# Optimization experiments

Hardware: AMD Instinct MI355X
Metric: run time of the kernel (lower is better)

## Reference

```python
import jax, jax.numpy as jnp
import numpy as np

EXPAND = 2  # expand_ratio: head dim


def setup_inputs() -> dict:
    key = jax.random.key(0)
    k1, k2, k3 = jax.random.split(key, 3)
    n, b, d = 4096, 8, 1024
    x = jax.random.normal(k1, (n, b, d), dtype=jnp.float32)
    lower_bound = jnp.zeros((d,), dtype=jnp.float32)
    W_in = jax.random.normal(k2, (d, 3 * d), dtype=jnp.float32) / np.sqrt(d)
    W_out = jax.random.normal(k3, (d, d), dtype=jnp.float32) / np.sqrt(d)
    return {"x": x, "lower_bound": lower_bound, "W_in": W_in, "W_out": W_out}


def reference(x, lower_bound, W_in, W_out):
    # x: (n, b, d) sequence-first
    n, b, d = x.shape
    e = EXPAND
    h = d // e
    feat = x @ W_in                                  # (n, b, 3d)
    V, Q, Fg = jnp.split(feat, 3, axis=-1)
    V = jax.nn.gelu(V, approximate=False)            # nn.GELU default = exact erf
    Q = jax.nn.gelu(Q, approximate=False)
    Fg = jax.nn.sigmoid(Fg)
    V = V.reshape(n, b, h, e)
    Q = Q.reshape(n, b, h, e)
    Fg = Fg.reshape(n, b, h, e)
    lb = lower_bound.reshape(h, e)
    lam = lb + (1.0 - lb) * Fg                       # decay gate in (lb, 1)
    K = 1.0 - lam
    # GLA recurrence: S_t = diag(lam_t) S_{t-1} + k_t v_t^T ; o_t = q_t S_t
    # (exp(log_lambda) == lambda, so log-space decay collapses to direct multiply)
    def step(S, inp):
        lam_t, k_t, v_t, q_t = inp                   # each (b, h, e)
        S = lam_t[..., :, None] * S + k_t[..., :, None] * v_t[..., None, :]
        o_t = jnp.einsum('bhk,bhkv->bhv', q_t, S)
        return S, o_t
    S0 = jnp.zeros((b, h, e, e), dtype=x.dtype)
    _, o = jax.lax.scan(step, S0, (lam, K, V, Q))    # o: (n, b, h, e)
    o = o.reshape(n, b, d)
    return o @ W_out
```

## Files before the change

kernel.cpp:

```cpp
#include <hip/hip_runtime.h>
#include <hip/hip_bf16.h>
#include <math.h>

using frag8 = __attribute__((ext_vector_type(8))) short;
using f32x4 = __attribute__((ext_vector_type(4))) float;

#define BM 256
#define BN 256

typedef const __attribute__((address_space(1))) unsigned char glb_u8;
typedef __attribute__((address_space(3))) unsigned char lds_u8;

__device__ __forceinline__ float b2f(unsigned short v) {
    union { unsigned u; float f; } x; x.u = ((unsigned)v) << 16; return x.f;
}
__device__ __forceinline__ unsigned short f2b(float f) {
    union { float f; unsigned u; } x; x.f = f;
    unsigned u = x.u;
    u += 0x7fffu + ((u >> 16) & 1u);
    return (unsigned short)(u >> 16);
}

__global__ __launch_bounds__(256) void cast_kernel(const float* __restrict__ in,
                                                   unsigned short* __restrict__ out, long n) {
    long i = ((long)blockIdx.x * 256 + threadIdx.x) * 8;
    if (i >= n) return;
    float4 a = *(const float4*)(in + i);
    float4 b = *(const float4*)(in + i + 4);
    struct alignas(16) U8 { unsigned short s[8]; } o;
    o.s[0] = f2b(a.x); o.s[1] = f2b(a.y); o.s[2] = f2b(a.z); o.s[3] = f2b(a.w);
    o.s[4] = f2b(b.x); o.s[5] = f2b(b.y); o.s[6] = f2b(b.z); o.s[7] = f2b(b.w);
    *(U8*)(out + i) = o;
}

__global__ void transpose_cast(const float* __restrict__ in, unsigned short* __restrict__ out,
                               int R, int Ccols) {
    __shared__ float tile[32][33];
    int bx = blockIdx.x * 32;
    int by = blockIdx.y * 32;
    int tx = threadIdx.x, ty = threadIdx.y;
    for (int r = ty; r < 32; r += 8)
        tile[r][tx] = in[(size_t)(by + r) * Ccols + bx + tx];
    __syncthreads();
    for (int r = ty; r < 32; r += 8)
        out[(size_t)(bx + r) * R + by + tx] = f2b(tile[tx][r]);
}

__global__ __launch_bounds__(512, 2) void gemm_bf16(
    const unsigned short* __restrict__ A, const unsigned short* __restrict__ Bt,
    int M, int N, int K, int mode,
    float* __restrict__ Cf,
    unsigned short* __restrict__ Vp, unsigned short* __restrict__ Qp,
    unsigned short* __restrict__ Lp, const float* __restrict__ lb) {
    __shared__ __align__(16) char smem[131072];

    const int tid = threadIdx.x;
    const int lane16 = tid & 15;
    const int quad = (tid >> 4) & 3;
    const int wave = tid >> 6;
    const int wm = wave >> 2;
    const int wn = wave & 3;

    const int nbx = N / BN;
    const int nwg = (int)gridDim.x;
    const int sw = ((int)blockIdx.x & 7) * (nwg >> 3) + ((int)blockIdx.x >> 3);
    const long m0 = (long)(sw / nbx) * BM;
    const long n0 = (long)(sw % nbx) * BN;
    const long K2 = (long)K * 2;

    const int c0 = (tid & 7) ^ ((tid >> 3) & 7);
    long srcL0, srcL1; int dstL0, dstL1;
    {
        const int kk2 = (c0 & 3) << 4;
        const int r0 = ((tid >> 3) << 1) + (c0 >> 2);
        const int r1 = ((64 + (tid >> 3)) << 1) + (c0 >> 2);
        srcL0 = (long)r0 * K2 + kk2;
        srcL1 = (long)r1 * K2 + kk2;
        dstL0 = tid * 16;
        dstL1 = 8192 + tid * 16;
    }
    const char* Ab = (const char*)A + m0 * K2;
    const char* Bb = (const char*)Bt + n0 * K2;

    int offA[8], offB[4];
#pragma unroll
    for (int mf = 0; mf < 8; ++mf) {
        int row = wm * 128 + mf * 16 + lane16;
        int line = row >> 1;
        int c = (((row & 1) << 2) | quad) ^ (line & 7);
        offA[mf] = line * 128 + c * 16;
    }
#pragma unroll
    for (int nf = 0; nf < 4; ++nf) {
        int row = wn * 64 + nf * 16 + lane16;
        int line = row >> 1;
        int c = (((row & 1) << 2) | quad) ^ (line & 7);
        offB[nf] = 16384 + line * 128 + c * 16;
    }

    f32x4 acc[8][4];
#pragma unroll
    for (int i = 0; i < 8; ++i)
#pragma unroll
        for (int j = 0; j < 4; ++j) acc[i][j] = (f32x4){0.f, 0.f, 0.f, 0.f};

#define STAGE(u) do { \
        char* ldb = smem + ((u) & 3) * 32768; \
        long kb = (long)(u) * 64; \
        __builtin_amdgcn_global_load_lds((glb_u8*)(Ab + srcL0 + kb), (lds_u8*)(ldb + dstL0), 16, 0, 0); \
        __builtin_amdgcn_global_load_lds((glb_u8*)(Ab + srcL1 + kb), (lds_u8*)(ldb + dstL1), 16, 0, 0); \
        __builtin_amdgcn_global_load_lds((glb_u8*)(Bb + srcL0 + kb), (lds_u8*)(ldb + 16384 + dstL0), 16, 0, 0); \
        __builtin_amdgcn_global_load_lds((glb_u8*)(Bb + srcL1 + kb), (lds_u8*)(ldb + 16384 + dstL1), 16, 0, 0); \
    } while (0)

    const int NT = K >> 5;
    STAGE(0); STAGE(1); STAGE(2);
    asm volatile("s_waitcnt vmcnt(8)" ::: "memory");
    __builtin_amdgcn_s_barrier();

    for (int t = 0; t < NT; ++t) {
        if (t + 3 < NT) STAGE(t + 3);
        const char* ub = smem + (t & 3) * 32768;
        frag8 bfr[4], af[4];
#pragma unroll
        for (int nf = 0; nf < 4; ++nf) bfr[nf] = *(const frag8*)(ub + offB[nf]);
#pragma unroll
        for (int mf = 0; mf < 4; ++mf) af[mf] = *(const frag8*)(ub + offA[mf]);
        __builtin_amdgcn_s_setprio(1);
#pragma unroll
        for (int mf = 0; mf < 4; ++mf)
#pragma unroll
            for (int nf = 0; nf < 4; ++nf)
                acc[mf][nf] = __builtin_amdgcn_mfma_f32_16x16x32_bf16(af[mf], bfr[nf], acc[mf][nf], 0, 0, 0);
        __builtin_amdgcn_s_setprio(0);
#pragma unroll
        for (int mf = 0; mf < 4; ++mf) af[mf] = *(const frag8*)(ub + offA[4 + mf]);
        __builtin_amdgcn_s_setprio(1);
#pragma unroll
        for (int mf = 0; mf < 4; ++mf)
#pragma unroll
            for (int nf = 0; nf < 4; ++nf)
                acc[4 + mf][nf] = __builtin_amdgcn_mfma_f32_16x16x32_bf16(af[mf], bfr[nf], acc[4 + mf][nf], 0, 0, 0);
        __builtin_amdgcn_s_setprio(0);
        if (t < NT - 3)       { asm volatile("s_waitcnt vmcnt(8)" ::: "memory"); }
        else if (t == NT - 3) { asm volatile("s_waitcnt vmcnt(4)" ::: "memory"); }
        else if (t == NT - 2) { asm volatile("s_waitcnt vmcnt(0)" ::: "memory"); }
        __builtin_amdgcn_s_barrier();
    }
#undef STAGE

    if (mode == 0) {
#pragma unroll
        for (int mf = 0; mf < 8; ++mf)
#pragma unroll
            for (int nf = 0; nf < 4; ++nf) {
                long col = n0 + wn * 64 + nf * 16 + lane16;
#pragma unroll
                for (int r = 0; r < 4; ++r) {
                    long row = m0 + wm * 128 + mf * 16 + quad * 4 + r;
                    Cf[row * N + col] = acc[mf][nf][r];
                }
            }
    } else {
        const int seg = (int)(n0 >> 10);
        const int cbase = (int)(n0 & 1023) + wn * 64;
        unsigned short* dst = (seg == 0) ? Vp : (seg == 1 ? Qp : Lp);
#pragma unroll
        for (int mf = 0; mf < 8; ++mf)
#pragma unroll
            for (int nf = 0; nf < 4; ++nf) {
                int col = cbase + nf * 16 + lane16;
#pragma unroll
                for (int r = 0; r < 4; ++r) {
                    long row = m0 + wm * 128 + mf * 16 + quad * 4 + r;
                    float v = acc[mf][nf][r];
                    float res;
                    if (seg < 2) {
                        float u = 1.59576912f * v * (1.0f + 0.044715f * v * v);
                        res = v / (1.0f + __expf(-u));
                    } else {
                        float sg = 1.0f / (1.0f + __expf(-v));
                        float l = lb[col];
                        res = l + (1.0f - l) * sg;
                    }
                    dst[row * 1024 + col] = f2b(res);
                }
            }
    }
}

__global__ __launch_bounds__(256) void scan_phase1(
    const unsigned short* __restrict__ lam, const unsigned short* __restrict__ V,
    float* __restrict__ Sl, float* __restrict__ P, int L) {
    int cid = blockIdx.x * 256 + threadIdx.x;
    int c = blockIdx.y;
    int bi = cid >> 9, h = cid & 511;
    float s00 = 0, s01 = 0, s10 = 0, s11 = 0, p0 = 1.f, p1 = 1.f;
    int t0 = c * L;
    const unsigned* lamp = (const unsigned*)lam;
    const unsigned* vp = (const unsigned*)V;
    for (int t = t0; t < t0 + L; ++t) {
        long idx = (long)(t * 8 + bi) * 512 + h;
        unsigned lu = lamp[idx], vu = vp[idx];
        float la0 = b2f((unsigned short)lu), la1 = b2f((unsigned short)(lu >> 16));
        float v0 = b2f((unsigned short)vu), v1 = b2f((unsigned short)(vu >> 16));
        float k0 = 1.f - la0, k1 = 1.f - la1;
        s00 = fmaf(la0, s00, k0 * v0); s01 = fmaf(la0, s01, k0 * v1);
        s10 = fmaf(la1, s10, k1 * v0); s11 = fmaf(la1, s11, k1 * v1);
        p0 *= la0; p1 *= la1;
    }
    long base = (long)c * 4096 + cid;
    ((float4*)Sl)[base] = make_float4(s00, s01, s10, s11);
    ((float2*)P)[base] = make_float2(p0, p1);
}

__global__ __launch_bounds__(256) void scan_phase2(
    const float* __restrict__ Sl, const float* __restrict__ P,
    float* __restrict__ Sini, int C) {
    int idx = blockIdx.x * 256 + threadIdx.x;
    int cid = idx >> 2, ij = idx & 3, i = (idx >> 1) & 1;
    float s = 0.f;
    for (int c = 0; c < C; ++c) {
        long base = (long)c * 4096 + cid;
        Sini[base * 4 + ij] = s;
        s = fmaf(P[base * 2 + i], s, Sl[base * 4 + ij]);
    }
}

__global__ __launch_bounds__(256) void scan_phase3(
    const unsigned short* __restrict__ lam, const unsigned short* __restrict__ V,
    const unsigned short* __restrict__ Q, const float* __restrict__ Sini,
    unsigned short* __restrict__ o, int L) {
    int cid = blockIdx.x * 256 + threadIdx.x;
    int c = blockIdx.y;
    int bi = cid >> 9, h = cid & 511;
    float4 si = ((const float4*)Sini)[(long)c * 4096 + cid];
    float s00 = si.x, s01 = si.y, s10 = si.z, s11 = si.w;
    int t0 = c * L;
    const unsigned* lamp = (const unsigned*)lam;
    const unsigned* vp = (const unsigned*)V;
    const unsigned* qp = (const unsigned*)Q;
    unsigned* op = (unsigned*)o;
    for (int t = t0; t < t0 + L; ++t) {
        long idx = (long)(t * 8 + bi) * 512 + h;
        unsigned lu = lamp[idx], vu = vp[idx], qu = qp[idx];
        float la0 = b2f((unsigned short)lu), la1 = b2f((unsigned short)(lu >> 16));
        float v0 = b2f((unsigned short)vu), v1 = b2f((unsigned short)(vu >> 16));
        float q0 = b2f((unsigned short)qu), q1 = b2f((unsigned short)(qu >> 16));
        float k0 = 1.f - la0, k1 = 1.f - la1;
        s00 = fmaf(la0, s00, k0 * v0); s01 = fmaf(la0, s01, k0 * v1);
        s10 = fmaf(la1, s10, k1 * v0); s11 = fmaf(la1, s11, k1 * v1);
        float o0 = q0 * s00 + q1 * s10;
        float o1 = q0 * s01 + q1 * s11;
        op[idx] = (unsigned)f2b(o0) | ((unsigned)f2b(o1) << 16);
    }
}

extern "C" void kernel_launch(void* const* d_in, const int* in_sizes, int n_in,
                              void* d_out, int out_size, void* d_ws, size_t ws_size,
                              hipStream_t stream) {
    const float* x = (const float*)d_in[0];
    const float* lb = (const float*)d_in[1];
    const float* W_in = (const float*)d_in[2];
    const float* W_out = (const float*)d_in[3];
    float* out = (float*)d_out;

    const int n = 4096, b = 8, d = 1024;
    const long NB = (long)n * b;
    const int C = 64, L = 64;

    char* ws = (char*)d_ws;
    size_t off = 0;
    auto alloc = [&](size_t bytes) -> char* {
        char* p = ws + off;
        off += (bytes + 255) & ~(size_t)255;
        return p;
    };
    unsigned short* xb   = (unsigned short*)alloc(NB * d * 2);
    unsigned short* Wint = (unsigned short*)alloc((size_t)3 * d * d * 2);
    unsigned short* Wot  = (unsigned short*)alloc((size_t)d * d * 2);
    unsigned short* Vb   = (unsigned short*)alloc(NB * d * 2);
    unsigned short* Qb   = (unsigned short*)alloc(NB * d * 2);
    unsigned short* Lb   = (unsigned short*)alloc(NB * d * 2);
    float* Sl   = (float*)alloc((size_t)C * 4096 * 4 * 4);
    float* P    = (float*)alloc((size_t)C * 4096 * 2 * 4);
    float* Sini = (float*)alloc((size_t)C * 4096 * 4 * 4);

    cast_kernel<<<dim3((unsigned)((NB * d) / (256 * 8))), 256, 0, stream>>>(x, xb, NB * d);
    transpose_cast<<<dim3(3 * d / 32, d / 32), dim3(32, 8), 0, stream>>>(W_in, Wint, d, 3 * d);
    transpose_cast<<<dim3(d / 32, d / 32), dim3(32, 8), 0, stream>>>(W_out, Wot, d, d);
    const int nwg1 = (3 * d / BN) * (int)(NB / BM);
    gemm_bf16<<<dim3(nwg1), 512, 0, stream>>>(
        xb, Wint, (int)NB, 3 * d, d, 1, nullptr, Vb, Qb, Lb, lb);
    scan_phase1<<<dim3(16, C), 256, 0, stream>>>(Lb, Vb, Sl, P, L);
    scan_phase2<<<dim3(64), 256, 0, stream>>>(Sl, P, Sini, C);
    unsigned short* ob = xb;
    scan_phase3<<<dim3(16, C), 256, 0, stream>>>(Lb, Vb, Qb, Sini, ob, L);
    const int nwg2 = (d / BN) * (int)(NB / BM);
    gemm_bf16<<<dim3(nwg2), 512, 0, stream>>>(
        ob, Wot, (int)NB, d, d, 0, out, nullptr, nullptr, nullptr, nullptr);
}
```

Measured before the change: 711.2 us.

## Restructure GEMM main loop into fine-grained 8-phase ping-pong schedule

Replaces the 4-stage K=32 LDS ring with two 64 KB buffers, each holding a K=64 tile split into A and B quarter-tiles. Loads are issued one quarter at a time, interleaved with LDS fragment reads and MFMA blocks separated by barriers. The loop is unrolled over K=128, and the LDS layout and swizzle change accordingly. The goal is finer overlap of global→LDS loads, LDS reads and MFMA, at the cost of many more barriers and an assumption that K is a multiple of 128.

```diff
diff --git a/kernel.cpp b/kernel.cpp
--- a/kernel.cpp
+++ b/kernel.cpp
@@ -68,86 +68,116 @@
     const long n0 = (long)(sw % nbx) * BN;
     const long K2 = (long)K * 2;
 
-    const int c0 = (tid & 7) ^ ((tid >> 3) & 7);
-    long srcL0, srcL1; int dstL0, dstL1;
-    {
-        const int kk2 = (c0 & 3) << 4;
-        const int r0 = ((tid >> 3) << 1) + (c0 >> 2);
-        const int r1 = ((64 + (tid >> 3)) << 1) + (c0 >> 2);
-        srcL0 = (long)r0 * K2 + kk2;
-        srcL1 = (long)r1 * K2 + kk2;
-        dstL0 = tid * 16;
-        dstL1 = 8192 + tid * 16;
-    }
+    const int c16 = (((tid & 7) ^ ((tid >> 3) & 7)) << 4);
+    const long o64 = 64 * K2, o128 = 128 * K2;
     const char* Ab = (const char*)A + m0 * K2;
     const char* Bb = (const char*)Bt + n0 * K2;
-
-    int offA[8], offB[4];
-#pragma unroll
-    for (int mf = 0; mf < 8; ++mf) {
-        int row = wm * 128 + mf * 16 + lane16;
-        int line = row >> 1;
-        int c = (((row & 1) << 2) | quad) ^ (line & 7);
-        offA[mf] = line * 128 + c * 16;
-    }
-#pragma unroll
-    for (int nf = 0; nf < 4; ++nf) {
-        int row = wn * 64 + nf * 16 + lane16;
-        int line = row >> 1;
-        int c = (((row & 1) << 2) | quad) ^ (line & 7);
-        offB[nf] = 16384 + line * 128 + c * 16;
-    }
+    const char* pA0 = Ab + (long)(tid >> 3) * K2 + c16;
+    const char* pA1 = pA0 + o128;
+    const char* pB0 = Bb + (long)(tid >> 3) * K2 + c16;
+    const char* pB1 = pB0 + o128;
+    const int dst0 = tid * 16;
+
+    const int baseA = wm * 16384 + lane16 * 128;
+    const int baseB = 32768 + (wn >> 1) * 16384 + (wn & 1) * 8192 + lane16 * 128;
+    const int swz0 = ((quad ^ (lane16 & 7)) << 4);
+    const int swz1 = (((4 + quad) ^ (lane16 & 7)) << 4);
 
     f32x4 acc[8][4];
 #pragma unroll
     for (int i = 0; i < 8; ++i)
 #pragma unroll
         for (int j = 0; j < 4; ++j) acc[i][j] = (f32x4){0.f, 0.f, 0.f, 0.f};
-
-#define STAGE(u) do { \
-        char* ldb = smem + ((u) & 3) * 32768; \
-        long kb = (long)(u) * 64; \
-        __builtin_amdgcn_global_load_lds((glb_u8*)(Ab + srcL0 + kb), (lds_u8*)(ldb + dstL0), 16, 0, 0); \
-        __builtin_amdgcn_global_load_lds((glb_u8*)(Ab + srcL1 + kb), (lds_u8*)(ldb + dstL1), 16, 0, 0); \
-        __builtin_amdgcn_global_load_lds((glb_u8*)(Bb + srcL0 + kb), (lds_u8*)(ldb + 16384 + dstL0), 16, 0, 0); \
-        __builtin_amdgcn_global_load_lds((glb_u8*)(Bb + srcL1 + kb), (lds_u8*)(ldb + 16384 + dstL1), 16, 0, 0); \
+    frag8 a0[4], a1[4], b0[4], b1[4];
+
+#define STAGE(P, R, KO) do { \
+        __builtin_amdgcn_global_load_lds((glb_u8*)((P) + (KO)), \
+            (lds_u8*)(smem + (R) + dst0), 16, 0, 0); \
+        __builtin_amdgcn_global_load_lds((glb_u8*)((P) + o64 + (KO)), \
+            (lds_u8*)(smem + (R) + 8192 + dst0), 16, 0, 0); \
     } while (0)
-
-    const int NT = K >> 5;
-    STAGE(0); STAGE(1); STAGE(2);
-    asm volatile("s_waitcnt vmcnt(8)" ::: "memory");
-    __builtin_amdgcn_s_barrier();
-
-    for (int t = 0; t < NT; ++t) {
-        if (t + 3 < NT) STAGE(t + 3);
-        const char* ub = smem + (t & 3) * 32768;
-        frag8 bfr[4], af[4];
-#pragma unroll
-        for (int nf = 0; nf < 4; ++nf) bfr[nf] = *(const frag8*)(ub + offB[nf]);
-#pragma unroll
-        for (int mf = 0; mf < 4; ++mf) af[mf] = *(const frag8*)(ub + offA[mf]);
-        __builtin_amdgcn_s_setprio(1);
-#pragma unroll
-        for (int mf = 0; mf < 4; ++mf)
-#pragma unroll
-            for (int nf = 0; nf < 4; ++nf)
-                acc[mf][nf] = __builtin_amdgcn_mfma_f32_16x16x32_bf16(af[mf], bfr[nf], acc[mf][nf], 0, 0, 0);
-        __builtin_amdgcn_s_setprio(0);
-#pragma unroll
-        for (int mf = 0; mf < 4; ++mf) af[mf] = *(const frag8*)(ub + offA[4 + mf]);
-        __builtin_amdgcn_s_setprio(1);
-#pragma unroll
-        for (int mf = 0; mf < 4; ++mf)
-#pragma unroll
-            for (int nf = 0; nf < 4; ++nf)
-                acc[4 + mf][nf] = __builtin_amdgcn_mfma_f32_16x16x32_bf16(af[mf], bfr[nf], acc[4 + mf][nf], 0, 0, 0);
-        __builtin_amdgcn_s_setprio(0);
-        if (t < NT - 3)       { asm volatile("s_waitcnt vmcnt(8)" ::: "memory"); }
-        else if (t == NT - 3) { asm volatile("s_waitcnt vmcnt(4)" ::: "memory"); }
-        else if (t == NT - 2) { asm volatile("s_waitcnt vmcnt(0)" ::: "memory"); }
-        __builtin_amdgcn_s_barrier();
-    }
+#define RD4(D, BUF, BASE, SW) do { \
+        D[0] = *(const frag8*)(smem + (BUF) + (BASE) + (SW)); \
+        D[1] = *(const frag8*)(smem + (BUF) + (BASE) + 2048 + (SW)); \
+        D[2] = *(const frag8*)(smem + (BUF) + (BASE) + 4096 + (SW)); \
+        D[3] = *(const frag8*)(smem + (BUF) + (BASE) + 6144 + (SW)); \
+    } while (0)
+#define MM(AF, BF, RO) do { \
+        _Pragma("unroll") \
+        for (int _m = 0; _m < 4; ++_m) \
+            _Pragma("unroll") \
+            for (int _n = 0; _n < 4; ++_n) \
+                acc[(RO) + _m][_n] = __builtin_amdgcn_mfma_f32_16x16x32_bf16( \
+                    AF[_m], BF[_n], acc[(RO) + _m][_n], 0, 0, 0); \
+    } while (0)
+#define VM2 asm volatile("s_waitcnt vmcnt(2)" ::: "memory")
+#define VM0 asm volatile("s_waitcnt vmcnt(0)" ::: "memory")
+#define BARR __builtin_amdgcn_s_barrier()
+#define PRIO1 __builtin_amdgcn_s_setprio(1)
+#define PRIO0 __builtin_amdgcn_s_setprio(0)
+
+    STAGE(pA0, 0, 0); STAGE(pA1, 16384, 0); STAGE(pB0, 32768, 0); STAGE(pB1, 49152, 0);
+    STAGE(pA0, 65536, 128);
+    VM2; BARR;
+    RD4(a0, 0, baseA, swz0); RD4(b0, 0, baseB, swz0);
+
+    long ko = 0;
+    const int NI = K >> 7;
+    for (int i = 0; i < NI - 1; ++i, ko += 256) {
+        STAGE(pA1, 65536 + 16384, ko + 128);
+        RD4(a1, 0, baseA + 8192, swz0);
+        BARR; PRIO1; MM(a0, b0, 0); PRIO0; BARR;
+        STAGE(pB0, 65536 + 32768, ko + 128);
+        RD4(a0, 0, baseA, swz1); RD4(b1, 0, baseB, swz1);
+        BARR; PRIO1; MM(a1, b0, 4); PRIO0; BARR;
+        STAGE(pB1, 65536 + 49152, ko + 128);
+        RD4(a1, 0, baseA + 8192, swz1);
+        BARR; PRIO1; MM(a0, b1, 0); PRIO0; BARR;
+        STAGE(pA0, 0, ko + 256);
+        VM2; BARR;
+        RD4(a0, 65536, baseA, swz0); RD4(b0, 65536, baseB, swz0);
+        PRIO1; MM(a1, b1, 4); PRIO0; BARR;
+        STAGE(pA1, 16384, ko + 256);
+        RD4(a1, 65536, baseA + 8192, swz0);
+        BARR; PRIO1; MM(a0, b0, 0); PRIO0; BARR;
+        STAGE(pB0, 32768, ko + 256);
+        RD4(a0, 65536, baseA, swz1); RD4(b1, 65536, baseB, swz1);
+        BARR; PRIO1; MM(a1, b0, 4); PRIO0; BARR;
+        STAGE(pB1, 49152, ko + 256);
+        RD4(a1, 65536, baseA + 8192, swz1);
+        BARR; PRIO1; MM(a0, b1, 0); PRIO0; BARR;
+        STAGE(pA0, 65536, ko + 384);
+        VM2; BARR;
+        RD4(a0, 0, baseA, swz0); RD4(b0, 0, baseB, swz0);
+        PRIO1; MM(a1, b1, 4); PRIO0; BARR;
+    }
+    STAGE(pA1, 65536 + 16384, ko + 128);
+    RD4(a1, 0, baseA + 8192, swz0);
+    BARR; PRIO1; MM(a0, b0, 0); PRIO0; BARR;
+    STAGE(pB0, 65536 + 32768, ko + 128);
+    RD4(a0, 0, baseA, swz1); RD4(b1, 0, baseB, swz1);
+    BARR; PRIO1; MM(a1, b0, 4); PRIO0; BARR;
+    STAGE(pB1, 65536 + 49152, ko + 128);
+    RD4(a1, 0, baseA + 8192, swz1);
+    BARR; PRIO1; MM(a0, b1, 0); PRIO0; BARR;
+    VM0; BARR;
+    RD4(a0, 65536, baseA, swz0); RD4(b0, 65536, baseB, swz0);
+    PRIO1; MM(a1, b1, 4); PRIO0; BARR;
+    RD4(a1, 65536, baseA + 8192, swz0);
+    BARR; PRIO1; MM(a0, b0, 0); PRIO0; BARR;
+    RD4(a0, 65536, baseA, swz1); RD4(b1, 65536, baseB, swz1);
+    BARR; PRIO1; MM(a1, b0, 4); PRIO0; BARR;
+    RD4(a1, 65536, baseA + 8192, swz1);
+    BARR; PRIO1; MM(a0, b1, 0); PRIO0; BARR;
+    PRIO1; MM(a1, b1, 4); PRIO0;
 #undef STAGE
+#undef RD4
+#undef MM
+#undef VM2
+#undef VM0
+#undef BARR
+#undef PRIO1
+#undef PRIO0
 
     if (mode == 0) {
 #pragma unroll
```

Measured after the change: 706.7 us. About the same (-0.6%).

## Restructure bf16 GEMM main loop into ping-pong register double-buffered schedule

Applied to the files above, without the earlier changes.

Rewrites the GEMM inner loop to process two K-steps per iteration. It splits the A and B global-to-LDS staging into separate phases and prefetches the next tile's A/B fragments into alternate register sets while MFMAs run on the current ones. It also changes the LDS layout to a simpler row-major tile with a 4-way XOR swizzle and precomputed base read offsets. The intent is to overlap LDS reads and global loads with MFMA work, at the cost of more barriers per step, higher register pressure, and a loop that assumes an even number of K steps.

```diff
diff --git a/kernel.cpp b/kernel.cpp
--- a/kernel.cpp
+++ b/kernel.cpp
@@ -55,8 +55,9 @@
     __shared__ __align__(16) char smem[131072];
 
     const int tid = threadIdx.x;
-    const int lane16 = tid & 15;
-    const int quad = (tid >> 4) & 3;
+    const int lane = tid & 63;
+    const int lane16 = lane & 15;
+    const int quad = lane >> 4;
     const int wave = tid >> 6;
     const int wm = wave >> 2;
     const int wn = wave & 3;
@@ -68,86 +69,105 @@
     const long n0 = (long)(sw % nbx) * BN;
     const long K2 = (long)K * 2;
 
-    const int c0 = (tid & 7) ^ ((tid >> 3) & 7);
-    long srcL0, srcL1; int dstL0, dstL1;
-    {
-        const int kk2 = (c0 & 3) << 4;
-        const int r0 = ((tid >> 3) << 1) + (c0 >> 2);
-        const int r1 = ((64 + (tid >> 3)) << 1) + (c0 >> 2);
-        srcL0 = (long)r0 * K2 + kk2;
-        srcL1 = (long)r1 * K2 + kk2;
-        dstL0 = tid * 16;
-        dstL1 = 8192 + tid * 16;
-    }
+    const int c0x16 = (((tid & 3) ^ ((tid >> 3) & 3)) << 4);
+    const long srcO0 = (long)(tid >> 2) * K2 + c0x16;
+    const long srcO1 = srcO0 + 128 * K2;
     const char* Ab = (const char*)A + m0 * K2;
     const char* Bb = (const char*)Bt + n0 * K2;
-
-    int offA[8], offB[4];
-#pragma unroll
-    for (int mf = 0; mf < 8; ++mf) {
-        int row = wm * 128 + mf * 16 + lane16;
-        int line = row >> 1;
-        int c = (((row & 1) << 2) | quad) ^ (line & 7);
-        offA[mf] = line * 128 + c * 16;
-    }
-#pragma unroll
-    for (int nf = 0; nf < 4; ++nf) {
-        int row = wn * 64 + nf * 16 + lane16;
-        int line = row >> 1;
-        int c = (((row & 1) << 2) | quad) ^ (line & 7);
-        offB[nf] = 16384 + line * 128 + c * 16;
-    }
+    const int dst0 = tid * 16;
+
+    const int swz = ((quad ^ ((lane16 >> 1) & 3)) << 4);
+    const int aRd = wm * 8192 + lane16 * 64 + swz;
+    const int bRd = 16384 + wn * 4096 + lane16 * 64 + swz;
 
     f32x4 acc[8][4];
 #pragma unroll
     for (int i = 0; i < 8; ++i)
 #pragma unroll
         for (int j = 0; j < 4; ++j) acc[i][j] = (f32x4){0.f, 0.f, 0.f, 0.f};
-
-#define STAGE(u) do { \
-        char* ldb = smem + ((u) & 3) * 32768; \
-        long kb = (long)(u) * 64; \
-        __builtin_amdgcn_global_load_lds((glb_u8*)(Ab + srcL0 + kb), (lds_u8*)(ldb + dstL0), 16, 0, 0); \
-        __builtin_amdgcn_global_load_lds((glb_u8*)(Ab + srcL1 + kb), (lds_u8*)(ldb + dstL1), 16, 0, 0); \
-        __builtin_amdgcn_global_load_lds((glb_u8*)(Bb + srcL0 + kb), (lds_u8*)(ldb + 16384 + dstL0), 16, 0, 0); \
-        __builtin_amdgcn_global_load_lds((glb_u8*)(Bb + srcL1 + kb), (lds_u8*)(ldb + 16384 + dstL1), 16, 0, 0); \
+    frag8 aL[4], aH[4], bE[4], bO[4];
+
+#define STAGE_A(u_) do { int _sb = ((u_) & 3) << 15; long _kb = (long)(u_) * 64; \
+        __builtin_amdgcn_global_load_lds((glb_u8*)(Ab + srcO0 + _kb), \
+            (lds_u8*)(smem + _sb + dst0), 16, 0, 0); \
+        __builtin_amdgcn_global_load_lds((glb_u8*)(Ab + srcO1 + _kb), \
+            (lds_u8*)(smem + _sb + 8192 + dst0), 16, 0, 0); \
     } while (0)
+#define STAGE_B(u_) do { int _sb = ((u_) & 3) << 15; long _kb = (long)(u_) * 64; \
+        __builtin_amdgcn_global_load_lds((glb_u8*)(Bb + srcO0 + _kb), \
+            (lds_u8*)(smem + _sb + 16384 + dst0), 16, 0, 0); \
+        __builtin_amdgcn_global_load_lds((glb_u8*)(Bb + srcO1 + _kb), \
+            (lds_u8*)(smem + _sb + 24576 + dst0), 16, 0, 0); \
+    } while (0)
+#define RD_ALO(D, u_) do { const char* _p = smem + (((u_) & 3) << 15) + aRd; \
+        D[0] = *(const frag8*)(_p);        D[1] = *(const frag8*)(_p + 1024); \
+        D[2] = *(const frag8*)(_p + 2048); D[3] = *(const frag8*)(_p + 3072); } while (0)
+#define RD_AHI(D, u_) do { const char* _p = smem + (((u_) & 3) << 15) + aRd + 4096; \
+        D[0] = *(const frag8*)(_p);        D[1] = *(const frag8*)(_p + 1024); \
+        D[2] = *(const frag8*)(_p + 2048); D[3] = *(const frag8*)(_p + 3072); } while (0)
+#define RD_B(D, u_) do { const char* _p = smem + (((u_) & 3) << 15) + bRd; \
+        D[0] = *(const frag8*)(_p);        D[1] = *(const frag8*)(_p + 1024); \
+        D[2] = *(const frag8*)(_p + 2048); D[3] = *(const frag8*)(_p + 3072); } while (0)
+#define MM4(AF, BF, RO) do { \
+        _Pragma("unroll") \
+        for (int _m = 0; _m < 4; ++_m) \
+            _Pragma("unroll") \
+            for (int _n = 0; _n < 4; ++_n) \
+                acc[(RO) + _m][_n] = __builtin_amdgcn_mfma_f32_16x16x32_bf16( \
+                    AF[_m], BF[_n], acc[(RO) + _m][_n], 0, 0, 0); \
+    } while (0)
+#define FENCE(x_) do { \
+        if ((x_) < NT - 3)       asm volatile("s_waitcnt vmcnt(8)" ::: "memory"); \
+        else if ((x_) == NT - 3) asm volatile("s_waitcnt vmcnt(4)" ::: "memory"); \
+        else                     asm volatile("s_waitcnt vmcnt(0)" ::: "memory"); \
+    } while (0)
+#define BARR __builtin_amdgcn_s_barrier()
+#define PRIO1 __builtin_amdgcn_s_setprio(1)
+#define PRIO0 __builtin_amdgcn_s_setprio(0)
 
     const int NT = K >> 5;
-    STAGE(0); STAGE(1); STAGE(2);
+
+    STAGE_A(0); STAGE_B(0); STAGE_A(1); STAGE_B(1); STAGE_A(2); STAGE_B(2);
     asm volatile("s_waitcnt vmcnt(8)" ::: "memory");
-    __builtin_amdgcn_s_barrier();
-
-    for (int t = 0; t < NT; ++t) {
-        if (t + 3 < NT) STAGE(t + 3);
-        const char* ub = smem + (t & 3) * 32768;
-        frag8 bfr[4], af[4];
-#pragma unroll
-        for (int nf = 0; nf < 4; ++nf) bfr[nf] = *(const frag8*)(ub + offB[nf]);
-#pragma unroll
-        for (int mf = 0; mf < 4; ++mf) af[mf] = *(const frag8*)(ub + offA[mf]);
-        __builtin_amdgcn_s_setprio(1);
-#pragma unroll
-        for (int mf = 0; mf < 4; ++mf)
-#pragma unroll
-            for (int nf = 0; nf < 4; ++nf)
-                acc[mf][nf] = __builtin_amdgcn_mfma_f32_16x16x32_bf16(af[mf], bfr[nf], acc[mf][nf], 0, 0, 0);
-        __builtin_amdgcn_s_setprio(0);
-#pragma unroll
-        for (int mf = 0; mf < 4; ++mf) af[mf] = *(const frag8*)(ub + offA[4 + mf]);
-        __builtin_amdgcn_s_setprio(1);
-#pragma unroll
-        for (int mf = 0; mf < 4; ++mf)
-#pragma unroll
-            for (int nf = 0; nf < 4; ++nf)
-                acc[4 + mf][nf] = __builtin_amdgcn_mfma_f32_16x16x32_bf16(af[mf], bfr[nf], acc[4 + mf][nf], 0, 0, 0);
-        __builtin_amdgcn_s_setprio(0);
-        if (t < NT - 3)       { asm volatile("s_waitcnt vmcnt(8)" ::: "memory"); }
-        else if (t == NT - 3) { asm volatile("s_waitcnt vmcnt(4)" ::: "memory"); }
-        else if (t == NT - 2) { asm volatile("s_waitcnt vmcnt(0)" ::: "memory"); }
-        __builtin_amdgcn_s_barrier();
-    }
-#undef STAGE
+    BARR;
+    RD_ALO(aL, 0); RD_B(bE, 0);
+
+    for (int u = 0; u < NT; u += 2) {
+        if (u + 3 < NT) STAGE_A(u + 3);
+        RD_AHI(aH, u);
+        BARR;
+        PRIO1; MM4(aL, bE, 0); PRIO0;
+        BARR;
+        if (u + 3 < NT) STAGE_B(u + 3);
+        {
+            FENCE(u); BARR;
+            RD_ALO(aL, u + 1); RD_B(bO, u + 1);
+        }
+        PRIO1; MM4(aH, bE, 4); PRIO0;
+        BARR;
+        if (u + 4 < NT) STAGE_A(u + 4);
+        RD_AHI(aH, u + 1);
+        BARR;
+        PRIO1; MM4(aL, bO, 0); PRIO0;
+        BARR;
+        if (u + 4 < NT) STAGE_B(u + 4);
+        if (u + 2 < NT) {
+            FENCE(u + 1); BARR;
+            RD_ALO(aL, u + 2); RD_B(bE, u + 2);
+        }
+        PRIO1; MM4(aH, bO, 4); PRIO0;
+        BARR;
+    }
+#undef STAGE_A
+#undef STAGE_B
+#undef RD_ALO
+#undef RD_AHI
+#undef RD_B
+#undef MM4
+#undef FENCE
+#undef BARR
+#undef PRIO1
+#undef PRIO0
 
     if (mode == 0) {
 #pragma unroll
```

Result: no change. 709.6 us (-0.2%).
